# Optimization experiments

Hardware: AMD Instinct MI355X
Metric: run time of the kernel (lower is better)

## Reference

```python
import jax, jax.numpy as jnp
import numpy as np

B, S, D, H, V = 32, 1024, 512, 4, 8185
DH = 3 * D // H  # 384 per-head projection; q/k/v each 128
FFN = 4 * D
LN_EPS = 1e-3  # keras LayerNormalization default epsilon


def _pos_encoding(seq_len, d_model):
    pos = np.arange(seq_len)[:, None].astype(np.float32)
    i = np.arange(d_model)[None, :].astype(np.float32)
    angles = pos / np.power(10000.0, 2.0 * (i // 2) / np.float32(d_model))
    angles[:, 0::2] = np.sin(angles[:, 0::2])
    angles[:, 1::2] = np.cos(angles[:, 1::2])
    return jnp.asarray(angles, dtype=jnp.float32)  # [S, D]


def _layernorm(x, g, b):
    mu = jnp.mean(x, axis=-1, keepdims=True)
    var = jnp.mean(jnp.square(x - mu), axis=-1, keepdims=True)
    return (x - mu) * jax.lax.rsqrt(var + LN_EPS) * g + b


def setup_inputs() -> dict:
    key = jax.random.key(0)
    ks = jax.random.split(key, 8)
    sc = 0.02
    return {
        "inputs": jax.random.randint(ks[0], (B, S), 0, V, dtype=jnp.int32),
        "emb": jax.random.normal(ks[1], (V, D), jnp.float32) * sc,
        "Wp": jax.random.normal(ks[2], (H, D, DH), jnp.float32) * sc,
        "bp": jnp.zeros((H, DH), jnp.float32),
        "Wo": jax.random.normal(ks[3], (D, D), jnp.float32) * sc,
        "bo": jnp.zeros((D,), jnp.float32),
        "ln1_g": jnp.ones((D,), jnp.float32),
        "ln1_b": jnp.zeros((D,), jnp.float32),
        "W1": jax.random.normal(ks[4], (D, FFN), jnp.float32) * sc,
        "b1": jnp.zeros((FFN,), jnp.float32),
        "W2": jax.random.normal(ks[5], (FFN, D), jnp.float32) * sc,
        "b2": jnp.zeros((D,), jnp.float32),
        "ln2_g": jnp.ones((D,), jnp.float32),
        "ln2_b": jnp.zeros((D,), jnp.float32),
        "Wh": jax.random.normal(ks[6], (D, D), jnp.float32) * sc,
        "bh": jnp.zeros((D,), jnp.float32),
        "Wf": jax.random.normal(ks[7], (D, 1), jnp.float32) * sc,
        "bf": jnp.zeros((1,), jnp.float32),
    }


def reference(inputs, emb, Wp, bp, Wo, bo, ln1_g, ln1_b, W1, b1, W2, b2,
              ln2_g, ln2_b, Wh, bh, Wf, bf):
    b, s = inputs.shape
    x = emb[inputs] + _pos_encoding(s, emb.shape[1])[None]  # [B,S,D]

    # decoder block: batched per-head projections (q|k|v packed along last axis)
    res = x
    d = jnp.einsum('bsd,hde->bhse', x, Wp) + bp[:, None, :]  # [B,H,S,3*dh]
    q, k, v = jnp.split(d, 3, axis=-1)  # each [B,H,S,dh]
    # NOTE: source scales by rsqrt(seq_len) (tf.shape(k)[1]), not head dim
    scale = jax.lax.rsqrt(jnp.float32(s))
    scores = jnp.einsum('bhse,bhte->bhst', q, k) * scale  # [B,H,S,S]
    heads = jnp.einsum('bhst,bhte->bhse', scores, v)  # linear attn (no softmax)
    concat = heads.transpose(0, 2, 1, 3).reshape(b, s, -1)  # [B,S,D]
    attn = concat @ Wo + bo
    x = _layernorm(attn + res, ln1_g, ln1_b)
    h = jax.nn.relu(x @ W1 + b1) @ W2 + b2
    x = _layernorm(h + x, ln2_g, ln2_b)

    # classification head on first token
    x0 = x[:, 0]
    hid = jax.nn.relu(x0 @ Wh + bh)
    logits = hid @ Wf + bf  # [B,1]
    return logits, jax.nn.sigmoid(logits)
```

## Files before the change

kernel.cpp:

```cpp
#include <hip/hip_runtime.h>
#include <hip/hip_bf16.h>

__global__ __launch_bounds__(512) void qr_k(
    const int* __restrict__ inp, const float* __restrict__ emb,
    const float* __restrict__ Wp, const float* __restrict__ bp,
    float* __restrict__ X0, float* __restrict__ r, float* __restrict__ alpha,
    float* __restrict__ Acc, int* __restrict__ Cnt)
{
    __shared__ float xs[512];
    __shared__ float red[512];
    __shared__ __align__(16) float q0s[128];
    int b = blockIdx.x, h = blockIdx.y, t = threadIdx.x;
    if (b == 0 && h == 0) {
        if (t < 32) Acc[t] = 0.f;
        else if (t < 64) Cnt[t - 32] = 0;
    }
    int tok0 = inp[b * 1024];
    {
        float v = emb[(long)tok0 * 512 + t] + ((t & 1) ? 1.0f : 0.0f);
        xs[t] = v;
        if (h == 0) X0[b * 512 + t] = v;
    }
    __syncthreads();

    int f = t & 127, dh = t >> 7;
    const float* wq = Wp + (long)h * 196608 + f;
    float acc = 0.f;
#pragma unroll 16
    for (int d = dh * 128; d < dh * 128 + 128; d++)
        acc += xs[d] * wq[(long)d * 384];
    red[t] = acc;
    __syncthreads();
    if (t < 128)
        q0s[t] = red[t] + red[t + 128] + red[t + 256] + red[t + 384]
               + bp[h * 384 + t];
    __syncthreads();
    if (t < 128) red[t] = q0s[t] * bp[h * 384 + 128 + t];
    __syncthreads();
    for (int w = 64; w >= 1; w >>= 1) {
        if (t < w) red[t] += red[t + w];
        __syncthreads();
    }
    if (t == 0) alpha[b * 4 + h] = red[0];

    const float4* q4 = (const float4*)q0s;
    {
        int d = t;
        const float4* wr = (const float4*)(Wp + ((long)(h * 512 + d)) * 384 + 128);
        float a2 = 0.f;
#pragma unroll 8
        for (int f4 = 0; f4 < 32; f4++) {
            float4 w = wr[f4], qq = q4[f4];
            a2 += w.x * qq.x + w.y * qq.y + w.z * qq.z + w.w * qq.w;
        }
        r[((long)(b * 4 + h)) * 512 + d] = a2;
    }
}

__global__ __launch_bounds__(256) void xu_k(
    const int* __restrict__ inp, const float* __restrict__ emb,
    const float* __restrict__ r, const float* __restrict__ alpha,
    float* __restrict__ Tpp, float* __restrict__ Gp)
{
    __shared__ float redT[4][4][64][8];
    __shared__ float redG[4][4];
    int b = blockIdx.x, sg = blockIdx.y, t = threadIdx.x;
    int wave = t >> 6, lane = t & 63;

    float rsv[4][8];
    float al[4];
#pragma unroll
    for (int h = 0; h < 4; h++) {
        const float4* rp = (const float4*)&r[((long)(b * 4 + h)) * 512 + lane * 8];
        float4 r0 = rp[0], r1 = rp[1];
        rsv[h][0] = r0.x; rsv[h][1] = r0.y; rsv[h][2] = r0.z; rsv[h][3] = r0.w;
        rsv[h][4] = r1.x; rsv[h][5] = r1.y; rsv[h][6] = r1.z; rsv[h][7] = r1.w;
        al[h] = alpha[b * 4 + h];
    }
    float w4[4];
#pragma unroll
    for (int j = 0; j < 4; j++) {
        float expo = (float)(lane * 8 + j * 2) * (1.0f / 512.0f);
        w4[j] = exp2f(-expo * 13.287712379549449f);
    }

    float accT[4][8] = {};
    float gacc[4] = {};
    int s0 = sg * 64 + wave * 16;
#pragma unroll
    for (int g = 0; g < 4; g++) {
        float xv[4][8];
        float up[4][4];
#pragma unroll
        for (int i = 0; i < 4; i++) {
            int srow = s0 + g * 4 + i;
            int tok = inp[b * 1024 + srow];
            const float4* e = (const float4*)&emb[(long)tok * 512 + lane * 8];
            float4 e0 = e[0], e1 = e[1];
            float sf = (float)srow;
            float sv[4], cv[4];
#pragma unroll
            for (int j = 0; j < 4; j++) {
                float ang = sf * w4[j];
                sv[j] = __sinf(ang);
                cv[j] = __cosf(ang);
            }
            xv[i][0] = e0.x + sv[0]; xv[i][1] = e0.y + cv[0];
            xv[i][2] = e0.z + sv[1]; xv[i][3] = e0.w + cv[1];
            xv[i][4] = e1.x + sv[2]; xv[i][5] = e1.y + cv[2];
            xv[i][6] = e1.z + sv[3]; xv[i][7] = e1.w + cv[3];
#pragma unroll
            for (int h = 0; h < 4; h++) {
                float acc = 0.f;
#pragma unroll
                for (int jj = 0; jj < 8; jj++) acc += xv[i][jj] * rsv[h][jj];
                up[i][h] = acc;
            }
        }
#pragma unroll
        for (int off = 32; off; off >>= 1) {
#pragma unroll
            for (int i = 0; i < 4; i++)
#pragma unroll
                for (int h = 0; h < 4; h++)
                    up[i][h] += __shfl_xor(up[i][h], off);
        }
#pragma unroll
        for (int i = 0; i < 4; i++) {
#pragma unroll
            for (int h = 0; h < 4; h++) {
                float u = up[i][h] + al[h];
                gacc[h] += u;
#pragma unroll
                for (int jj = 0; jj < 8; jj++) accT[h][jj] += u * xv[i][jj];
            }
        }
    }
#pragma unroll
    for (int h = 0; h < 4; h++) {
        *(float4*)&redT[wave][h][lane][0] =
            make_float4(accT[h][0], accT[h][1], accT[h][2], accT[h][3]);
        *(float4*)&redT[wave][h][lane][4] =
            make_float4(accT[h][4], accT[h][5], accT[h][6], accT[h][7]);
    }
    if (lane == 0) {
#pragma unroll
        for (int h = 0; h < 4; h++) redG[wave][h] = gacc[h];
    }
    __syncthreads();
    long base = (long)(b * 16 + sg) * 2048;
#pragma unroll
    for (int k = 0; k < 8; k++) {
        int idx = t + k * 256;
        int h = idx >> 9, d = idx & 511;
        float v = redT[0][h][d >> 3][d & 7] + redT[1][h][d >> 3][d & 7]
                + redT[2][h][d >> 3][d & 7] + redT[3][h][d >> 3][d & 7];
        Tpp[base + idx] = v;
    }
    if (t < 4) Gp[(b * 16 + sg) * 4 + t] =
        redG[0][t] + redG[1][t] + redG[2][t] + redG[3][t];
}

__global__ __launch_bounds__(512) void att1_k(
    const float* __restrict__ Tpp, const float* __restrict__ Gp,
    const float* __restrict__ Wp, const float* __restrict__ bp,
    float* __restrict__ C0)
{
    __shared__ float tps[512];
    __shared__ float red[512];
    int b = blockIdx.x, jt = blockIdx.y, t = threadIdx.x;
    int h = jt >> 1, e0 = (jt & 1) * 64;
    {
        float v = 0.f;
#pragma unroll 8
        for (int sg = 0; sg < 16; sg++)
            v += Tpp[(long)b * 32768 + sg * 2048 + h * 512 + t];
        tps[t] = v;
    }
    __syncthreads();
    int e = e0 + (t & 63), rg = t >> 6;
    const float* wv = Wp + (long)h * 196608 + 256 + e;
    float acc = 0.f;
#pragma unroll 16
    for (int d = rg * 64; d < rg * 64 + 64; d++)
        acc += tps[d] * wv[(long)d * 384];
    red[t] = acc;
    __syncthreads();
    if (t < 64) {
        float gam = 0.f;
#pragma unroll
        for (int sg = 0; sg < 16; sg++) gam += Gp[(b * 16 + sg) * 4 + h];
        float sum = red[t] + red[t + 64] + red[t + 128] + red[t + 192]
                  + red[t + 256] + red[t + 320] + red[t + 384] + red[t + 448];
        float c = 0.03125f * (sum + gam * bp[h * 384 + 256 + e0 + t]);
        C0[b * 512 + h * 128 + e0 + t] = c;
    }
}

__global__ __launch_bounds__(512) void att2s_k(
    const float* __restrict__ C0, const float* __restrict__ Wo,
    const float* __restrict__ bo, const float* __restrict__ X0,
    float* __restrict__ A1, float* __restrict__ Stat)
{
    __shared__ float c0s[512];
    __shared__ float red[512];
    int b = blockIdx.x, jt = blockIdx.y, t = threadIdx.x;
    c0s[t] = C0[b * 512 + t];
    __syncthreads();
    int j = jt * 64 + (t & 63), rg = t >> 6;
    float acc = 0.f;
#pragma unroll 16
    for (int d = rg * 64; d < rg * 64 + 64; d++)
        acc += c0s[d] * Wo[(long)d * 512 + j];
    red[t] = acc;
    __syncthreads();
    if (t < 64) {
        int jj = jt * 64 + t;
        float a = red[t] + red[t + 64] + red[t + 128] + red[t + 192]
                + red[t + 256] + red[t + 320] + red[t + 384] + red[t + 448]
                + bo[jj] + X0[b * 512 + jj];
        A1[b * 512 + jj] = a;
        float s = a, q = a * a;
#pragma unroll
        for (int off = 32; off; off >>= 1) {
            s += __shfl_down(s, off);
            q += __shfl_down(q, off);
        }
        if (t == 0) {
            Stat[(b * 8 + jt) * 2]     = s;
            Stat[(b * 8 + jt) * 2 + 1] = q;
        }
    }
}

__global__ __launch_bounds__(256) void ffn1_k(
    const float* __restrict__ A1, const float* __restrict__ Stat,
    const float* __restrict__ g1, const float* __restrict__ b1v,
    const float* __restrict__ W1, float* __restrict__ Hp1)
{
    __shared__ float at[32][32];
    __shared__ float mrs[32][2];
    int jt = blockIdx.x, ks = blockIdx.y, t = threadIdx.x;
    if (t < 32) {
        float s = 0.f, q = 0.f;
#pragma unroll
        for (int p8 = 0; p8 < 8; p8++) {
            s += Stat[(t * 8 + p8) * 2];
            q += Stat[(t * 8 + p8) * 2 + 1];
        }
        float mean = s * (1.0f / 512.0f);
        float var = q * (1.0f / 512.0f) - mean * mean;
        mrs[t][0] = mean;
        mrs[t][1] = rsqrtf(var + 0.001f);
    }
    __syncthreads();
    {
        int row = t >> 3, f4 = t & 7;
        int col = ks * 32 + f4 * 4;
        float4 a4 = *(const float4*)&A1[(long)row * 512 + col];
        float4 g4 = *(const float4*)&g1[col];
        float4 bb = *(const float4*)&b1v[col];
        float mean = mrs[row][0], rstd = mrs[row][1];
        float4 v;
        v.x = (a4.x - mean) * rstd * g4.x + bb.x;
        v.y = (a4.y - mean) * rstd * g4.y + bb.y;
        v.z = (a4.z - mean) * rstd * g4.z + bb.z;
        v.w = (a4.w - mean) * rstd * g4.w + bb.w;
        ((float4*)at)[t] = v;
    }
    __syncthreads();
    int j = jt * 64 + (t & 63), rg = t >> 6;
    float acc[8] = {};
    const float* wp = W1 + (long)(ks * 32) * 2048 + j;
#pragma unroll 16
    for (int k = 0; k < 32; k++) {
        float wv = wp[(long)k * 2048];
#pragma unroll
        for (int rr = 0; rr < 8; rr++)
            acc[rr] += at[rg * 8 + rr][k] * wv;
    }
#pragma unroll
    for (int rr = 0; rr < 8; rr++)
        Hp1[((long)(ks * 32 + rg * 8 + rr)) * 2048 + j] = acc[rr];
}

__global__ __launch_bounds__(256) void ffn2_k(
    const float* __restrict__ Hp1, const float* __restrict__ b1,
    const float* __restrict__ W2, float* __restrict__ Hp2)
{
    __shared__ float at[32][32];
    int jt = blockIdx.x, ks2 = blockIdx.y, t = threadIdx.x;
    {
        int row = t >> 3, f4 = t & 7;
        int col4 = ks2 * 8 + f4;
        float4 v = ((const float4*)b1)[col4];
#pragma unroll
        for (int p = 0; p < 16; p++) {
            float4 pv = ((const float4*)Hp1)[(long)p * 16384 + row * 512 + col4];
            v.x += pv.x; v.y += pv.y; v.z += pv.z; v.w += pv.w;
        }
        v.x = fmaxf(v.x, 0.f); v.y = fmaxf(v.y, 0.f);
        v.z = fmaxf(v.z, 0.f); v.w = fmaxf(v.w, 0.f);
        ((float4*)at)[t] = v;
    }
    __syncthreads();
    int j = jt * 64 + (t & 63), rg = t >> 6;
    float acc[8] = {};
    const float* wp = W2 + (long)(ks2 * 32) * 512 + j;
#pragma unroll 16
    for (int k = 0; k < 32; k++) {
        float wv = wp[(long)k * 512];
#pragma unroll
        for (int rr = 0; rr < 8; rr++)
            acc[rr] += at[rg * 8 + rr][k] * wv;
    }
#pragma unroll
    for (int rr = 0; rr < 8; rr++)
        Hp2[((long)(ks2 * 32 + rg * 8 + rr)) * 512 + j] = acc[rr];
}

__global__ __launch_bounds__(512) void headp3_k(
    const float* __restrict__ Hp2, const float* __restrict__ b2,
    const float* __restrict__ A1, const float* __restrict__ Stat,
    const float* __restrict__ g1v, const float* __restrict__ b1v,
    const float* __restrict__ g2v, const float* __restrict__ b2v,
    const float* __restrict__ Wh, const float* __restrict__ bh,
    const float* __restrict__ Wf, const float* __restrict__ bf,
    float* __restrict__ Acc, int* __restrict__ Cnt, float* __restrict__ out)
{
    __shared__ float xs[512];
    __shared__ float red[512];
    __shared__ float sd[16];
    __shared__ float mr[2];
    int b = blockIdx.x, jt = blockIdx.y, t = threadIdx.x;
    int wave = t >> 6;
    if (t == 0) {
        float s = 0.f, q = 0.f;
#pragma unroll
        for (int p8 = 0; p8 < 8; p8++) {
            s += Stat[(b * 8 + p8) * 2];
            q += Stat[(b * 8 + p8) * 2 + 1];
        }
        float mean = s * (1.0f / 512.0f);
        mr[0] = mean;
        mr[1] = rsqrtf(q * (1.0f / 512.0f) - mean * mean + 0.001f);
    }
    __syncthreads();
    float mean1 = mr[0], rstd1 = mr[1];
    float v;
    {
        float y1 = (A1[b * 512 + t] - mean1) * rstd1 * g1v[t] + b1v[t];
        v = b2[t] + y1;
#pragma unroll 16
        for (int ks = 0; ks < 64; ks++)
            v += Hp2[((long)(ks * 32 + b)) * 512 + t];
    }
    float s = v;
#pragma unroll
    for (int off = 32; off; off >>= 1) s += __shfl_down(s, off);
    if ((t & 63) == 0) sd[wave] = s;
    __syncthreads();
    float mean = (sd[0] + sd[1] + sd[2] + sd[3]
                + sd[4] + sd[5] + sd[6] + sd[7]) * (1.0f / 512.0f);
    float d0 = v - mean;
    float v2 = d0 * d0;
#pragma unroll
    for (int off = 32; off; off >>= 1) v2 += __shfl_down(v2, off);
    if ((t & 63) == 0) sd[8 + wave] = v2;
    __syncthreads();
    float var = (sd[8] + sd[9] + sd[10] + sd[11]
               + sd[12] + sd[13] + sd[14] + sd[15]) * (1.0f / 512.0f);
    float rstd = rsqrtf(var + 0.001f);
    xs[t] = d0 * rstd * g2v[t] + b2v[t];
    __syncthreads();

    int j = jt * 64 + (t & 63), rg = t >> 6;
    const float* w = Wh + j;
    float acc = 0.f;
#pragma unroll 16
    for (int d = rg * 64; d < rg * 64 + 64; d++)
        acc += xs[d] * w[(long)d * 512];
    red[t] = acc;
    __syncthreads();
    if (t < 64) {
        int jj = jt * 64 + t;
        float hid = red[t] + red[t + 64] + red[t + 128] + red[t + 192]
                  + red[t + 256] + red[t + 320] + red[t + 384] + red[t + 448]
                  + bh[jj];
        hid = fmaxf(hid, 0.f);
        float p = hid * Wf[jj];
#pragma unroll
        for (int off = 32; off; off >>= 1) p += __shfl_down(p, off);
        if (t == 0) {
            atomicAdd(&Acc[b], p);
            __threadfence();
            int old = atomicAdd(&Cnt[b], 1);
            if (old == 7) {
                float tot = atomicAdd(&Acc[b], 0.0f);
                float logit = tot + bf[0];
                out[b] = logit;
                out[32 + b] = 1.f / (1.f + expf(-logit));
            }
        }
    }
}

extern "C" void kernel_launch(void* const* d_in, const int* in_sizes, int n_in,
                              void* d_out, int out_size, void* d_ws, size_t ws_size,
                              hipStream_t stream)
{
    const int*   inputs = (const int*)  d_in[0];
    const float* emb    = (const float*)d_in[1];
    const float* Wp     = (const float*)d_in[2];
    const float* bp     = (const float*)d_in[3];
    const float* Wo     = (const float*)d_in[4];
    const float* bo     = (const float*)d_in[5];
    const float* ln1_g  = (const float*)d_in[6];
    const float* ln1_b  = (const float*)d_in[7];
    const float* W1     = (const float*)d_in[8];
    const float* b1     = (const float*)d_in[9];
    const float* W2     = (const float*)d_in[10];
    const float* b2     = (const float*)d_in[11];
    const float* ln2_g  = (const float*)d_in[12];
    const float* ln2_b  = (const float*)d_in[13];
    const float* Wh     = (const float*)d_in[14];
    const float* bh     = (const float*)d_in[15];
    const float* Wf     = (const float*)d_in[16];
    const float* bf     = (const float*)d_in[17];
    float* out = (float*)d_out;

    char* p = (char*)d_ws;
    float* X0    = (float*)p;  p += 65536;
    float* r     = (float*)p;  p += 262144;
    float* alpha = (float*)p;  p += 1024;
    float* Gp    = (float*)p;  p += 8192;
    float* Tpp   = (float*)p;  p += 4194304;
    float* C0    = (float*)p;  p += 65536;
    float* A1    = (float*)p;  p += 65536;
    float* Stat  = (float*)p;  p += 2048;
    float* Acc   = (float*)p;  p += 512;
    int*   Cnt   = (int*)p;    p += 512;
    float* Hp1   = (float*)p;  p += 4194304;
    float* Hp2   = (float*)p;  p += 4194304;

    qr_k<<<dim3(32, 4), 512, 0, stream>>>(inputs, emb, Wp, bp, X0, r, alpha,
                                          Acc, Cnt);
    xu_k<<<dim3(32, 16), 256, 0, stream>>>(inputs, emb, r, alpha, Tpp, Gp);
    att1_k<<<dim3(32, 8), 512, 0, stream>>>(Tpp, Gp, Wp, bp, C0);
    att2s_k<<<dim3(32, 8), 512, 0, stream>>>(C0, Wo, bo, X0, A1, Stat);
    ffn1_k<<<dim3(32, 16), 256, 0, stream>>>(A1, Stat, ln1_g, ln1_b, W1, Hp1);
    ffn2_k<<<dim3(8, 64), 256, 0, stream>>>(Hp1, b1, W2, Hp2);
    headp3_k<<<dim3(32, 8), 512, 0, stream>>>(Hp2, b2, A1, Stat,
                                              ln1_g, ln1_b, ln2_g, ln2_b,
                                              Wh, bh, Wf, bf, Acc, Cnt, out);
}
```

Baseline: 166.9 us.

## Fuse attention value and output projections into one kernel with 1024-thread blocks

Merges att1_k and att2s_k into a single att12_k kernel. Each block recomputes the full context vector C0 for all heads in shared memory and then applies Wo, so the C0 round trip through global memory and one launch go away. qr_k and headp3_k move to 1024-thread blocks that split their reduction loops in half for more parallelism per block. In exchange, every jt block now redoes the whole Wv projection (8x redundant work and Wp reads), and the larger blocks may lower occupancy.

```diff
diff --git a/kernel.cpp b/kernel.cpp
--- a/kernel.cpp
+++ b/kernel.cpp
@@ -1,14 +1,14 @@
 #include <hip/hip_runtime.h>
 #include <hip/hip_bf16.h>
 
-__global__ __launch_bounds__(512) void qr_k(
+__global__ __launch_bounds__(1024) void qr_k(
     const int* __restrict__ inp, const float* __restrict__ emb,
     const float* __restrict__ Wp, const float* __restrict__ bp,
     float* __restrict__ X0, float* __restrict__ r, float* __restrict__ alpha,
     float* __restrict__ Acc, int* __restrict__ Cnt)
 {
     __shared__ float xs[512];
-    __shared__ float red[512];
+    __shared__ float red[1024];
     __shared__ __align__(16) float q0s[128];
     int b = blockIdx.x, h = blockIdx.y, t = threadIdx.x;
     if (b == 0 && h == 0) {
@@ -16,7 +16,7 @@
         else if (t < 64) Cnt[t - 32] = 0;
     }
     int tok0 = inp[b * 1024];
-    {
+    if (t < 512) {
         float v = emb[(long)tok0 * 512 + t] + ((t & 1) ? 1.0f : 0.0f);
         xs[t] = v;
         if (h == 0) X0[b * 512 + t] = v;
@@ -27,12 +27,13 @@
     const float* wq = Wp + (long)h * 196608 + f;
     float acc = 0.f;
 #pragma unroll 16
-    for (int d = dh * 128; d < dh * 128 + 128; d++)
+    for (int d = dh * 64; d < dh * 64 + 64; d++)
         acc += xs[d] * wq[(long)d * 384];
     red[t] = acc;
     __syncthreads();
     if (t < 128)
         q0s[t] = red[t] + red[t + 128] + red[t + 256] + red[t + 384]
+               + red[t + 512] + red[t + 640] + red[t + 768] + red[t + 896]
                + bp[h * 384 + t];
     __syncthreads();
     if (t < 128) red[t] = q0s[t] * bp[h * 384 + 128 + t];
@@ -44,17 +45,18 @@
     if (t == 0) alpha[b * 4 + h] = red[0];
 
     const float4* q4 = (const float4*)q0s;
-    {
-        int d = t;
-        const float4* wr = (const float4*)(Wp + ((long)(h * 512 + d)) * 384 + 128);
-        float a2 = 0.f;
-#pragma unroll 8
-        for (int f4 = 0; f4 < 32; f4++) {
-            float4 w = wr[f4], qq = q4[f4];
-            a2 += w.x * qq.x + w.y * qq.y + w.z * qq.z + w.w * qq.w;
-        }
-        r[((long)(b * 4 + h)) * 512 + d] = a2;
-    }
+    int d = t & 511, half = t >> 9;
+    const float4* wr = (const float4*)
+        (Wp + ((long)(h * 512 + d)) * 384 + 128 + half * 64);
+    float a2 = 0.f;
+#pragma unroll 16
+    for (int f4 = 0; f4 < 16; f4++) {
+        float4 w = wr[f4], qq = q4[half * 16 + f4];
+        a2 += w.x * qq.x + w.y * qq.y + w.z * qq.z + w.w * qq.w;
+    }
+    red[t] = a2;
+    __syncthreads();
+    if (t < 512) r[((long)(b * 4 + h)) * 512 + t] = red[t] + red[t + 512];
 }
 
 __global__ __launch_bounds__(256) void xu_k(
@@ -161,64 +163,62 @@
         redG[0][t] + redG[1][t] + redG[2][t] + redG[3][t];
 }
 
-__global__ __launch_bounds__(512) void att1_k(
+__global__ __launch_bounds__(1024) void att12_k(
     const float* __restrict__ Tpp, const float* __restrict__ Gp,
     const float* __restrict__ Wp, const float* __restrict__ bp,
-    float* __restrict__ C0)
-{
-    __shared__ float tps[512];
-    __shared__ float red[512];
+    const float* __restrict__ Wo, const float* __restrict__ bo,
+    const float* __restrict__ X0,
+    float* __restrict__ A1, float* __restrict__ Stat)
+{
+    __shared__ float tps[2048];
+    __shared__ float c0s[512];
+    __shared__ float red[1024];
+    __shared__ float gams[4];
     int b = blockIdx.x, jt = blockIdx.y, t = threadIdx.x;
-    int h = jt >> 1, e0 = (jt & 1) * 64;
+#pragma unroll
+    for (int i = 0; i < 2; i++) {
+        int idx = t + i * 1024;
+        float v = 0.f;
+#pragma unroll 16
+        for (int sg = 0; sg < 16; sg++)
+            v += Tpp[(long)b * 32768 + sg * 2048 + idx];
+        tps[idx] = v;
+    }
+    if (t < 4) {
+        float g = 0.f;
+#pragma unroll
+        for (int sg = 0; sg < 16; sg++) g += Gp[(b * 16 + sg) * 4 + t];
+        gams[t] = g;
+    }
+    __syncthreads();
+
     {
-        float v = 0.f;
-#pragma unroll 8
-        for (int sg = 0; sg < 16; sg++)
-            v += Tpp[(long)b * 32768 + sg * 2048 + h * 512 + t];
-        tps[t] = v;
-    }
-    __syncthreads();
-    int e = e0 + (t & 63), rg = t >> 6;
-    const float* wv = Wp + (long)h * 196608 + 256 + e;
-    float acc = 0.f;
-#pragma unroll 16
-    for (int d = rg * 64; d < rg * 64 + 64; d++)
-        acc += tps[d] * wv[(long)d * 384];
-    red[t] = acc;
-    __syncthreads();
-    if (t < 64) {
-        float gam = 0.f;
-#pragma unroll
-        for (int sg = 0; sg < 16; sg++) gam += Gp[(b * 16 + sg) * 4 + h];
-        float sum = red[t] + red[t + 64] + red[t + 128] + red[t + 192]
-                  + red[t + 256] + red[t + 320] + red[t + 384] + red[t + 448];
-        float c = 0.03125f * (sum + gam * bp[h * 384 + 256 + e0 + t]);
-        C0[b * 512 + h * 128 + e0 + t] = c;
-    }
-}
-
-__global__ __launch_bounds__(512) void att2s_k(
-    const float* __restrict__ C0, const float* __restrict__ Wo,
-    const float* __restrict__ bo, const float* __restrict__ X0,
-    float* __restrict__ A1, float* __restrict__ Stat)
-{
-    __shared__ float c0s[512];
-    __shared__ float red[512];
-    int b = blockIdx.x, jt = blockIdx.y, t = threadIdx.x;
-    c0s[t] = C0[b * 512 + t];
-    __syncthreads();
+        int out = t >> 1, halfc = t & 1;
+        int hh = out >> 7, e = out & 127;
+        const float* wv = Wp + (long)hh * 196608 + 256 + e;
+        const float* tp = tps + hh * 512;
+        float acc = 0.f;
+#pragma unroll 16
+        for (int d = halfc * 256; d < halfc * 256 + 256; d++)
+            acc += tp[d] * wv[(long)d * 384];
+        acc += __shfl_xor(acc, 1);
+        if (halfc == 0)
+            c0s[out] = 0.03125f * (acc + gams[hh] * bp[hh * 384 + 256 + e]);
+    }
+    __syncthreads();
+
     int j = jt * 64 + (t & 63), rg = t >> 6;
-    float acc = 0.f;
-#pragma unroll 16
-    for (int d = rg * 64; d < rg * 64 + 64; d++)
-        acc += c0s[d] * Wo[(long)d * 512 + j];
-    red[t] = acc;
+    float a2 = 0.f;
+#pragma unroll 16
+    for (int d = rg * 32; d < rg * 32 + 32; d++)
+        a2 += c0s[d] * Wo[(long)d * 512 + j];
+    red[t] = a2;
     __syncthreads();
     if (t < 64) {
         int jj = jt * 64 + t;
-        float a = red[t] + red[t + 64] + red[t + 128] + red[t + 192]
-                + red[t + 256] + red[t + 320] + red[t + 384] + red[t + 448]
-                + bo[jj] + X0[b * 512 + jj];
+        float a = bo[jj] + X0[b * 512 + jj];
+#pragma unroll
+        for (int k = 0; k < 16; k++) a += red[t + k * 64];
         A1[b * 512 + jj] = a;
         float s = a, q = a * a;
 #pragma unroll
@@ -319,7 +319,7 @@
         Hp2[((long)(ks2 * 32 + rg * 8 + rr)) * 512 + j] = acc[rr];
 }
 
-__global__ __launch_bounds__(512) void headp3_k(
+__global__ __launch_bounds__(1024) void headp3_k(
     const float* __restrict__ Hp2, const float* __restrict__ b2,
     const float* __restrict__ A1, const float* __restrict__ Stat,
     const float* __restrict__ g1v, const float* __restrict__ b1v,
@@ -329,11 +329,10 @@
     float* __restrict__ Acc, int* __restrict__ Cnt, float* __restrict__ out)
 {
     __shared__ float xs[512];
-    __shared__ float red[512];
+    __shared__ float red[1024];
     __shared__ float sd[16];
     __shared__ float mr[2];
     int b = blockIdx.x, jt = blockIdx.y, t = threadIdx.x;
-    int wave = t >> 6;
     if (t == 0) {
         float s = 0.f, q = 0.f;
 #pragma unroll
@@ -347,46 +346,51 @@
     }
     __syncthreads();
     float mean1 = mr[0], rstd1 = mr[1];
-    float v;
     {
-        float y1 = (A1[b * 512 + t] - mean1) * rstd1 * g1v[t] + b1v[t];
-        v = b2[t] + y1;
-#pragma unroll 16
-        for (int ks = 0; ks < 64; ks++)
-            v += Hp2[((long)(ks * 32 + b)) * 512 + t];
-    }
-    float s = v;
+        int j = t & 511, half = t >> 9;
+        float v = 0.f;
+#pragma unroll 16
+        for (int ks = half * 32; ks < half * 32 + 32; ks++)
+            v += Hp2[((long)(ks * 32 + b)) * 512 + j];
+        if (half == 0)
+            v += b2[j] + (A1[b * 512 + j] - mean1) * rstd1 * g1v[j] + b1v[j];
+        red[t] = v;
+    }
+    __syncthreads();
+    float a = 0.f;
+    if (t < 512) a = red[t] + red[t + 512];
+    float s = a;
 #pragma unroll
     for (int off = 32; off; off >>= 1) s += __shfl_down(s, off);
-    if ((t & 63) == 0) sd[wave] = s;
+    if (t < 512 && (t & 63) == 0) sd[t >> 6] = s;
     __syncthreads();
     float mean = (sd[0] + sd[1] + sd[2] + sd[3]
                 + sd[4] + sd[5] + sd[6] + sd[7]) * (1.0f / 512.0f);
-    float d0 = v - mean;
+    float d0 = a - mean;
     float v2 = d0 * d0;
 #pragma unroll
     for (int off = 32; off; off >>= 1) v2 += __shfl_down(v2, off);
-    if ((t & 63) == 0) sd[8 + wave] = v2;
+    if (t < 512 && (t & 63) == 0) sd[8 + (t >> 6)] = v2;
     __syncthreads();
     float var = (sd[8] + sd[9] + sd[10] + sd[11]
                + sd[12] + sd[13] + sd[14] + sd[15]) * (1.0f / 512.0f);
     float rstd = rsqrtf(var + 0.001f);
-    xs[t] = d0 * rstd * g2v[t] + b2v[t];
-    __syncthreads();
-
-    int j = jt * 64 + (t & 63), rg = t >> 6;
-    const float* w = Wh + j;
+    if (t < 512) xs[t] = d0 * rstd * g2v[t] + b2v[t];
+    __syncthreads();
+
+    int j2 = jt * 64 + (t & 63), rg = t >> 6;
+    const float* w = Wh + j2;
     float acc = 0.f;
 #pragma unroll 16
-    for (int d = rg * 64; d < rg * 64 + 64; d++)
+    for (int d = rg * 32; d < rg * 32 + 32; d++)
         acc += xs[d] * w[(long)d * 512];
     red[t] = acc;
     __syncthreads();
     if (t < 64) {
         int jj = jt * 64 + t;
-        float hid = red[t] + red[t + 64] + red[t + 128] + red[t + 192]
-                  + red[t + 256] + red[t + 320] + red[t + 384] + red[t + 448]
-                  + bh[jj];
+        float hid = bh[jj];
+#pragma unroll
+        for (int k = 0; k < 16; k++) hid += red[t + k * 64];
         hid = fmaxf(hid, 0.f);
         float p = hid * Wf[jj];
 #pragma unroll
@@ -435,7 +439,6 @@
     float* alpha = (float*)p;  p += 1024;
     float* Gp    = (float*)p;  p += 8192;
     float* Tpp   = (float*)p;  p += 4194304;
-    float* C0    = (float*)p;  p += 65536;
     float* A1    = (float*)p;  p += 65536;
     float* Stat  = (float*)p;  p += 2048;
     float* Acc   = (float*)p;  p += 512;
@@ -443,14 +446,14 @@
     float* Hp1   = (float*)p;  p += 4194304;
     float* Hp2   = (float*)p;  p += 4194304;
 
-    qr_k<<<dim3(32, 4), 512, 0, stream>>>(inputs, emb, Wp, bp, X0, r, alpha,
-                                          Acc, Cnt);
+    qr_k<<<dim3(32, 4), 1024, 0, stream>>>(inputs, emb, Wp, bp, X0, r, alpha,
+                                           Acc, Cnt);
     xu_k<<<dim3(32, 16), 256, 0, stream>>>(inputs, emb, r, alpha, Tpp, Gp);
-    att1_k<<<dim3(32, 8), 512, 0, stream>>>(Tpp, Gp, Wp, bp, C0);
-    att2s_k<<<dim3(32, 8), 512, 0, stream>>>(C0, Wo, bo, X0, A1, Stat);
+    att12_k<<<dim3(32, 8), 1024, 0, stream>>>(Tpp, Gp, Wp, bp, Wo, bo, X0,
+                                              A1, Stat);
     ffn1_k<<<dim3(32, 16), 256, 0, stream>>>(A1, Stat, ln1_g, ln1_b, W1, Hp1);
     ffn2_k<<<dim3(8, 64), 256, 0, stream>>>(Hp1, b1, W2, Hp2);
-    headp3_k<<<dim3(32, 8), 512, 0, stream>>>(Hp2, b2, A1, Stat,
-                                              ln1_g, ln1_b, ln2_g, ln2_b,
-                                              Wh, bh, Wf, bf, Acc, Cnt, out);
-}
+    headp3_k<<<dim3(32, 8), 1024, 0, stream>>>(Hp2, b2, A1, Stat,
+                                               ln1_g, ln1_b, ln2_g, ln2_b,
+                                               Wh, bh, Wf, bf, Acc, Cnt, out);
+}
```

Result: slower. 194.0 us (+16.2%).
